# Kernel tuning notes

Measured on AMD Instinct MI355X. Metric: run time of the kernel, lower is better.

## Reference

```python
import jax, jax.numpy as jnp
import numpy as np

D_MODEL = 1024
N_HEADS = 16
HEAD_DIM = D_MODEL // N_HEADS
B, S = 4, 2048


def setup_inputs() -> dict:
    key = jax.random.key(0)
    ks = jax.random.split(key, 12)
    s = 1.0 / np.sqrt(D_MODEL)
    inp = {
        'query': jax.random.normal(ks[0], (B, S, D_MODEL), jnp.float32),
        'key': jax.random.normal(ks[1], (B, S, D_MODEL), jnp.float32),
        'value': jax.random.normal(ks[2], (B, S, D_MODEL), jnp.float32),
        # causal mask, broadcast over batch and heads: [1,1,S,S]
        'mask': jnp.tril(jnp.ones((S, S), jnp.int32))[None, None],
        'Wq': jax.random.normal(ks[3], (D_MODEL, D_MODEL), jnp.float32) * s,
        'bq': jnp.zeros((D_MODEL,), jnp.float32),
        'Wk': jax.random.normal(ks[4], (D_MODEL, D_MODEL), jnp.float32) * s,
        'bk': jnp.zeros((D_MODEL,), jnp.float32),
        'Wv': jax.random.normal(ks[5], (D_MODEL, D_MODEL), jnp.float32) * s,
        'bv': jnp.zeros((D_MODEL,), jnp.float32),
        'Wo': jax.random.normal(ks[6], (D_MODEL, D_MODEL), jnp.float32) * s,
        'bo': jnp.zeros((D_MODEL,), jnp.float32),
    }
    return inp


def reference(query, key, value, mask, Wq, bq, Wk, bk, Wv, bv, Wo, bo):
    b, q_len, _ = query.shape
    scale = jnp.sqrt(jnp.float32(HEAD_DIM))
    # projections
    q = query @ Wq + bq
    k = key @ Wk + bk
    v = value @ Wv + bv
    # [b, h, s, hd]
    q = q.reshape(b, q_len, N_HEADS, HEAD_DIM).transpose(0, 2, 1, 3)
    k = k.reshape(b, -1, N_HEADS, HEAD_DIM).transpose(0, 2, 1, 3)
    v = v.reshape(b, -1, N_HEADS, HEAD_DIM).transpose(0, 2, 1, 3)
    scores = jnp.einsum('bhqd,bhkd->bhqk', q, k) / scale
    scores = jnp.where(mask == 0, jnp.float32(-jnp.inf), scores)
    attn = jax.nn.softmax(scores, axis=-1)  # dropout p=0 / eval mode
    out = jnp.einsum('bhqk,bhkd->bhqd', attn, v)
    out = out.transpose(0, 2, 1, 3).reshape(b, q_len, D_MODEL)
    return out @ Wo + bo
```

## Files before the change

kernel.cpp:

```cpp
#include <hip/hip_runtime.h>
#include <hip/hip_bf16.h>

typedef __attribute__((ext_vector_type(8))) short short8;
typedef __attribute__((ext_vector_type(4))) float floatx4;
typedef __attribute__((ext_vector_type(4))) unsigned short ushort4v;

#define D_MODEL 1024
#define S_LEN   2048
#define N_HEADS 16
#define HEAD_DIM 64
#define BATCH   4

__device__ __forceinline__ unsigned short f2bf(float x) {
    union { float f; unsigned int u; } v; v.f = x;
    unsigned int u = v.u;
    unsigned int r = (u + 0x7FFFu + ((u >> 16) & 1u)) >> 16;
    return (unsigned short)r;
}
__device__ __forceinline__ unsigned short f2bf_trunc(float x) {
    union { float f; unsigned int u; } v; v.f = x;
    return (unsigned short)(v.u >> 16);
}

__device__ __forceinline__ void gload_lds16(const void* g, void* s) {
    __builtin_amdgcn_global_load_lds(
        (const __attribute__((address_space(1))) void*)g,
        (__attribute__((address_space(3))) void*)s, 16, 0, 0);
}

struct Conv3 {
    const float* src[3];
    unsigned short* dst[3];
};

__global__ __launch_bounds__(256) void conv_bf16(Conv3 a) {
    const float* s = a.src[blockIdx.z];
    unsigned short* d = a.dst[blockIdx.z];
    size_t i = ((size_t)blockIdx.x * 256 + threadIdx.x) * 8;
    float4 f0 = *(const float4*)(s + i);
    float4 f1 = *(const float4*)(s + i + 4);
    short8 v;
    v[0] = (short)f2bf(f0.x); v[1] = (short)f2bf(f0.y);
    v[2] = (short)f2bf(f0.z); v[3] = (short)f2bf(f0.w);
    v[4] = (short)f2bf(f1.x); v[5] = (short)f2bf(f1.y);
    v[6] = (short)f2bf(f1.z); v[7] = (short)f2bf(f1.w);
    *(short8*)(d + i) = v;
}

struct Trans4 {
    const float* W[4];
    unsigned short* Wt[4];
};

__global__ __launch_bounds__(256) void transpose_w(Trans4 args) {
    __shared__ unsigned short tile[32][33];
    const float* W = args.W[blockIdx.z];
    unsigned short* Wt = args.Wt[blockIdx.z];
    int n0 = blockIdx.x * 32;
    int k0 = blockIdx.y * 32;
    int t = threadIdx.x;
    int r = t >> 5, c = t & 31;
    for (int i = 0; i < 4; ++i) {
        int k = k0 + r + i * 8;
        tile[r + i * 8][c] = f2bf(W[(size_t)k * D_MODEL + n0 + c]);
    }
    __syncthreads();
    for (int i = 0; i < 4; ++i) {
        int n = n0 + r + i * 8;
        Wt[(size_t)n * D_MODEL + k0 + c] = tile[c][r + i * 8];
    }
}

struct GemmIn {
    const unsigned short* A;
    const unsigned short* Bt;
    const float* bias;
    void* C;
    int mode;
};
struct Gemm3 { GemmIn g[3]; };

#define BAR()   asm volatile("s_barrier" ::: "memory")
#define LGKM0() asm volatile("s_waitcnt lgkmcnt(0)" ::: "memory")
#define VMW0()  asm volatile("s_waitcnt vmcnt(0)" ::: "memory")

#define READ_A4(BUF)                                                           \
    _Pragma("unroll") for (int ii = 0; ii < 4; ++ii) {                         \
        aF[ii][0] = *(const short8*)&lds[(BUF)*16384 + aOff + ii*512];         \
        aF[ii][1] = *(const short8*)&lds[(BUF)*16384 + aOff + ii*512 + 4096];  \
    }
#define READ_B2(BUF, J0, DST)                                                  \
    _Pragma("unroll") for (int jj = 0; jj < 2; ++jj) {                         \
        DST[jj][0] = *(const short8*)&lds[(BUF)*16384 + bOff + ((J0)+jj)*512]; \
        DST[jj][1] = *(const short8*)&lds[(BUF)*16384 + bOff + ((J0)+jj)*512 + 4096]; \
    }
#define MFMA_H(J0, BREG)                                                       \
    __builtin_amdgcn_s_setprio(1);                                             \
    _Pragma("unroll") for (int ii = 0; ii < 4; ++ii)                           \
    _Pragma("unroll") for (int jj = 0; jj < 2; ++jj) {                         \
        acc[ii][(J0)+jj] = __builtin_amdgcn_mfma_f32_16x16x32_bf16(            \
            aF[ii][0], BREG[jj][0], acc[ii][(J0)+jj], 0, 0, 0);                \
        acc[ii][(J0)+jj] = __builtin_amdgcn_mfma_f32_16x16x32_bf16(            \
            aF[ii][1], BREG[jj][1], acc[ii][(J0)+jj], 0, 0, 0);                \
    }                                                                          \
    __builtin_amdgcn_s_setprio(0)

__global__ __launch_bounds__(256, 2) void gemm_128(Gemm3 args) {
    constexpr int K = D_MODEL, N = D_MODEL;
    constexpr int NT = K / 64;
    constexpr int NI = NT / 2;
    GemmIn g = args.g[blockIdx.z];

    __shared__ __align__(16) unsigned short lds[32768];

    const int m0 = blockIdx.x * 128;
    const int n0 = blockIdx.y * 128;
    const int t = threadIdx.x;
    const int w = t >> 6, lane = t & 63;
    const int quad = lane >> 4, l16 = lane & 15;
    const int wm = w >> 1, wn = w & 1;

    const int srow = w * 32 + (lane >> 2);
    const int scol = ((lane & 3) * 8) ^ ((lane & 32) ? 16 : 0);

    const int fx = (quad * 8) ^ ((l16 & 8) ? 16 : 0);
    const int aOff = (wm * 64 + l16) * 32 + fx;
    const int bOff = 8192 + (wn * 64 + l16) * 32 + fx;

    floatx4 acc[4][4] = {};
    short8 aF[4][2], bE[2][2], bO[2][2];

    auto stageA = [&](int buf, int kt) {
        const unsigned short* s0 = g.A + (size_t)(m0 + srow) * K + kt * 64 + scol;
        unsigned short* d0 = &lds[buf * 16384 + (w * 32) * 32];
        gload_lds16(s0, d0);
        gload_lds16(s0 + 32, d0 + 4096);
        gload_lds16(s0 + (size_t)16 * K, d0 + 512);
        gload_lds16(s0 + (size_t)16 * K + 32, d0 + 512 + 4096);
    };
    auto stageB = [&](int buf, int kt) {
        const unsigned short* s0 = g.Bt + (size_t)(n0 + srow) * K + kt * 64 + scol;
        unsigned short* d0 = &lds[buf * 16384 + 8192 + (w * 32) * 32];
        gload_lds16(s0, d0);
        gload_lds16(s0 + 32, d0 + 4096);
        gload_lds16(s0 + (size_t)16 * K, d0 + 512);
        gload_lds16(s0 + (size_t)16 * K + 32, d0 + 512 + 4096);
    };

    stageA(0, 0); stageB(0, 0);
    VMW0();
    BAR();

    for (int n = 0; n < NI - 1; ++n) {
        const int t0 = 2 * n;
        READ_A4(0); READ_B2(0, 0, bE);
        stageB(1, t0 + 1);
        BAR(); LGKM0();
        MFMA_H(0, bE);
        BAR();
        READ_B2(0, 2, bO);
        stageA(1, t0 + 1);
        BAR(); LGKM0();
        MFMA_H(2, bO);
        VMW0();
        BAR();
        READ_A4(1); READ_B2(1, 0, bE);
        stageB(0, t0 + 2);
        BAR(); LGKM0();
        MFMA_H(0, bE);
        BAR();
        READ_B2(1, 2, bO);
        stageA(0, t0 + 2);
        BAR(); LGKM0();
        MFMA_H(2, bO);
        VMW0();
        BAR();
    }

    {
        READ_A4(0); READ_B2(0, 0, bE);
        stageB(1, NT - 1);
        BAR(); LGKM0();
        MFMA_H(0, bE);
        BAR();
        READ_B2(0, 2, bO);
        stageA(1, NT - 1);
        BAR(); LGKM0();
        MFMA_H(2, bO);
        VMW0();
        BAR();
        READ_A4(1); READ_B2(1, 0, bE);
        BAR(); LGKM0();
        MFMA_H(0, bE);
        BAR();
        READ_B2(1, 2, bO);
        LGKM0();
        MFMA_H(2, bO);
    }

    if (g.mode == 2) {
        unsigned short* Ct = (unsigned short*)g.C;
#pragma unroll
        for (int j = 0; j < 4; ++j) {
            int col = n0 + wn * 64 + j * 16 + l16;
            int h = col >> 6, dd = col & 63;
            float bv = g.bias[col];
#pragma unroll
            for (int i = 0; i < 4; ++i) {
                int row0 = m0 + wm * 64 + i * 16 + quad * 4;
                int bb = row0 >> 11, s = row0 & 2047;
                ushort4v u;
#pragma unroll
                for (int r = 0; r < 4; ++r) u[r] = f2bf(acc[i][j][r] + bv);
                *(ushort4v*)(Ct + ((size_t)(bb * 16 + h) * 64 + dd) * 2048 + s) = u;
            }
        }
    } else {
#pragma unroll
        for (int j = 0; j < 4; ++j) {
            int col = n0 + wn * 64 + j * 16 + l16;
            float bv = g.bias[col];
#pragma unroll
            for (int i = 0; i < 4; ++i) {
#pragma unroll
                for (int r = 0; r < 4; ++r) {
                    int row = m0 + wm * 64 + i * 16 + quad * 4 + r;
                    float v = acc[i][j][r] + bv;
                    if (g.mode == 1)
                        ((float*)g.C)[(size_t)row * N + col] = v;
                    else
                        ((unsigned short*)g.C)[(size_t)row * N + col] = f2bf(v);
                }
            }
        }
    }
}

__global__ __launch_bounds__(512) void flash_attn(
    const unsigned short* __restrict__ Qp,
    const unsigned short* __restrict__ Kp,
    const unsigned short* __restrict__ Vtg,
    unsigned short* __restrict__ Op) {
    constexpr int S = S_LEN, D = D_MODEL;
    __shared__ __align__(16) unsigned short Ks[64 * 64];
    __shared__ __align__(16) unsigned short Vs[64 * 64];
    __shared__ __align__(16) unsigned short Ps[8][16][72];

    int pair = blockIdx.x;
    int bh = blockIdx.y;
    int b = bh >> 4;
    int t = threadIdx.x;
    int wave = t >> 6, lane = t & 63;
    int quad = lane >> 4, l16 = lane & 15;

    const size_t head_off = (size_t)b * S * D + (size_t)(bh & 15) * HEAD_DIM;
    const unsigned short* Khead = Kp + head_off;
    const unsigned short* Vhead = Vtg + (size_t)bh * 64 * S;

    int q0l = pair * 128, q0h = (15 - pair) * 128;
    int qgl = q0l + wave * 16 + l16;
    int qgh = q0h + wave * 16 + l16;

    const unsigned short* qpl = Qp + head_off + (size_t)qgl * D + quad * 8;
    short8 ql0 = *(const short8*)qpl, ql1 = *(const short8*)(qpl + 32);
    const unsigned short* qph = Qp + head_off + (size_t)qgh * D + quad * 8;
    short8 qh0 = *(const short8*)qph, qh1 = *(const short8*)(qph + 32);

    floatx4 ol[4] = {}, oh[4] = {};
    float ll = 0.f, lh = 0.f;
    const float cs = 0.125f * 1.44269504088896340736f;

    int sw = wave & 3;
    bool doK = wave < 4;
    int srow = sw * 16 + (lane >> 2);
    int scol = (lane & 3) * 8;
    unsigned short* sdst0 = (doK ? Ks : Vs) + sw * 512;
    unsigned short* sdst1 = sdst0 + 2048;

    int wqminl = q0l + wave * 16, wqmaxl = wqminl + 15;
    int wqminh = q0h + wave * 16, wqmaxh = wqminh + 15;

    auto half_step = [&](int k0, int qg, int wqmin, float& l_i,
                         floatx4* o, short8 qb0, short8 qb1) {
        floatx4 st[4];
        for (int gk = 0; gk < 4; ++gk) {
            short8 ka0 = *(const short8*)&Ks[(gk * 16 + l16) * 32 + quad * 8];
            short8 ka1 = *(const short8*)&Ks[2048 + (gk * 16 + l16) * 32 + quad * 8];
            floatx4 s = {};
            s = __builtin_amdgcn_mfma_f32_16x16x32_bf16(ka0, qb0, s, 0, 0, 0);
            s = __builtin_amdgcn_mfma_f32_16x16x32_bf16(ka1, qb1, s, 0, 0, 0);
            st[gk] = s;
        }

        float sv[16];
        float rs = 0.f;
        if (k0 + 63 < wqmin) {
            for (int i = 0; i < 16; ++i) {
                sv[i] = __builtin_amdgcn_exp2f(st[i >> 2][i & 3] * cs);
                rs += sv[i];
            }
        } else {
            for (int gk = 0; gk < 4; ++gk)
                for (int r = 0; r < 4; ++r) {
                    int key = k0 + gk * 16 + quad * 4 + r;
                    float p = (key <= qg)
                        ? __builtin_amdgcn_exp2f(st[gk][r] * cs) : 0.f;
                    sv[gk * 4 + r] = p;
                    rs += p;
                }
        }
        rs += __shfl_xor(rs, 16);
        rs += __shfl_xor(rs, 32);
        l_i += rs;

        for (int gk = 0; gk < 4; ++gk) {
            ushort4v u;
            for (int r = 0; r < 4; ++r) u[r] = f2bf_trunc(sv[gk * 4 + r]);
            *(ushort4v*)&Ps[wave][l16][gk * 16 + quad * 4] = u;
        }

        short8 pf0 = *(const short8*)&Ps[wave][l16][quad * 8];
        short8 pf1 = *(const short8*)&Ps[wave][l16][32 + quad * 8];
        for (int jd = 0; jd < 4; ++jd) {
            short8 va0 = *(const short8*)&Vs[(jd * 16 + l16) * 32 + quad * 8];
            short8 va1 = *(const short8*)&Vs[2048 + (jd * 16 + l16) * 32 + quad * 8];
            o[jd] = __builtin_amdgcn_mfma_f32_16x16x32_bf16(va0, pf0, o[jd], 0, 0, 0);
            o[jd] = __builtin_amdgcn_mfma_f32_16x16x32_bf16(va1, pf1, o[jd], 0, 0, 0);
        }
    };

    int n_kt = 2 * (15 - pair) + 2;
    for (int kt = 0; kt < n_kt; ++kt) {
        int k0 = kt * 64;
        if (doK) {
            gload_lds16(Khead + (size_t)(k0 + srow) * D + scol, sdst0);
            gload_lds16(Khead + (size_t)(k0 + srow) * D + 32 + scol, sdst1);
        } else {
            gload_lds16(Vhead + (size_t)srow * S + k0 + scol, sdst0);
            gload_lds16(Vhead + (size_t)srow * S + k0 + 32 + scol, sdst1);
        }
        __syncthreads();

        if (k0 <= wqmaxl) half_step(k0, qgl, wqminl, ll, ol, ql0, ql1);
        if (k0 <= wqmaxh) half_step(k0, qgh, wqminh, lh, oh, qh0, qh1);
        __syncthreads();
    }

    {
        float inv = 1.0f / ll;
        unsigned short* op = Op + head_off + (size_t)qgl * D;
        for (int jd = 0; jd < 4; ++jd) {
            ushort4v u;
            for (int r = 0; r < 4; ++r) u[r] = f2bf(ol[jd][r] * inv);
            *(ushort4v*)(op + jd * 16 + quad * 4) = u;
        }
    }
    {
        float inv = 1.0f / lh;
        unsigned short* op = Op + head_off + (size_t)qgh * D;
        for (int jd = 0; jd < 4; ++jd) {
            ushort4v u;
            for (int r = 0; r < 4; ++r) u[r] = f2bf(oh[jd][r] * inv);
            *(ushort4v*)(op + jd * 16 + quad * 4) = u;
        }
    }
}

extern "C" void kernel_launch(void* const* d_in, const int* in_sizes, int n_in,
                              void* d_out, int out_size, void* d_ws,
                              size_t ws_size, hipStream_t stream) {
    const float* query = (const float*)d_in[0];
    const float* key   = (const float*)d_in[1];
    const float* value = (const float*)d_in[2];
    const float* Wq = (const float*)d_in[4];
    const float* bq = (const float*)d_in[5];
    const float* Wk = (const float*)d_in[6];
    const float* bk = (const float*)d_in[7];
    const float* Wv = (const float*)d_in[8];
    const float* bv = (const float*)d_in[9];
    const float* Wo = (const float*)d_in[10];
    const float* bo = (const float*)d_in[11];
    float* out = (float*)d_out;

    char* ws = (char*)d_ws;
    const size_t WT_SZ = (size_t)D_MODEL * D_MODEL * 2;
    const size_t X_SZ = (size_t)BATCH * S_LEN * D_MODEL * 2;
    unsigned short* wtq = (unsigned short*)(ws);
    unsigned short* wtk = (unsigned short*)(ws + WT_SZ);
    unsigned short* wtv = (unsigned short*)(ws + 2 * WT_SZ);
    unsigned short* wto = (unsigned short*)(ws + 3 * WT_SZ);
    unsigned short* Qbf = (unsigned short*)(ws + 4 * WT_SZ);
    unsigned short* Kbf = (unsigned short*)(ws + 4 * WT_SZ + X_SZ);
    unsigned short* Vbf = (unsigned short*)(ws + 4 * WT_SZ + 2 * X_SZ);
    unsigned short* Qp  = (unsigned short*)(ws + 4 * WT_SZ + 3 * X_SZ);
    unsigned short* Kp  = (unsigned short*)(ws + 4 * WT_SZ + 4 * X_SZ);
    unsigned short* Vtg = (unsigned short*)(ws + 4 * WT_SZ + 5 * X_SZ);
    unsigned short* Ao  = Qbf;

    Trans4 ta;
    ta.W[0] = Wq; ta.W[1] = Wk; ta.W[2] = Wv; ta.W[3] = Wo;
    ta.Wt[0] = wtq; ta.Wt[1] = wtk; ta.Wt[2] = wtv; ta.Wt[3] = wto;
    transpose_w<<<dim3(32, 32, 4), 256, 0, stream>>>(ta);

    Conv3 ca;
    ca.src[0] = query; ca.src[1] = key; ca.src[2] = value;
    ca.dst[0] = Qbf;   ca.dst[1] = Kbf; ca.dst[2] = Vbf;
    conv_bf16<<<dim3(4096, 1, 3), 256, 0, stream>>>(ca);

    Gemm3 gq;
    gq.g[0].A = Qbf; gq.g[0].Bt = wtq; gq.g[0].bias = bq; gq.g[0].C = Qp;  gq.g[0].mode = 0;
    gq.g[1].A = Kbf; gq.g[1].Bt = wtk; gq.g[1].bias = bk; gq.g[1].C = Kp;  gq.g[1].mode = 0;
    gq.g[2].A = Vbf; gq.g[2].Bt = wtv; gq.g[2].bias = bv; gq.g[2].C = Vtg; gq.g[2].mode = 2;
    gemm_128<<<dim3(64, 8, 3), 256, 0, stream>>>(gq);

    flash_attn<<<dim3(8, BATCH * N_HEADS), 512, 0, stream>>>(
        Qp, Kp, Vtg, Ao);

    Gemm3 go;
    go.g[0].A = Ao; go.g[0].Bt = wto; go.g[0].bias = bo; go.g[0].C = out; go.g[0].mode = 1;
    gemm_128<<<dim3(64, 8, 1), 256, 0, stream>>>(go);
}
```

Before: 329.8 us.

## Double-buffer K/V tiles in flash attention with swizzled LDS layout

Splits the K/V LDS staging into two buffers so the global-to-LDS load of the next key tile is issued before computing on the current one, waiting with a partial vmcnt instead of a full sync. Adds an XOR swizzle to the K, V and P LDS layouts to reduce bank conflicts, and raises wave priority around the MFMA blocks. The cost is double the K/V LDS footprint, which may lower occupancy. The swizzle has to match between the staging writes and the fragment reads, so any mismatch would give wrong results.

```diff
diff --git a/kernel.cpp b/kernel.cpp
--- a/kernel.cpp
+++ b/kernel.cpp
@@ -82,6 +82,7 @@
 
 #define BAR()   asm volatile("s_barrier" ::: "memory")
 #define LGKM0() asm volatile("s_waitcnt lgkmcnt(0)" ::: "memory")
+#define VMW2()  asm volatile("s_waitcnt vmcnt(2)" ::: "memory")
 #define VMW0()  asm volatile("s_waitcnt vmcnt(0)" ::: "memory")
 
 #define READ_A4(BUF)                                                           \
@@ -242,9 +243,9 @@
     const unsigned short* __restrict__ Vtg,
     unsigned short* __restrict__ Op) {
     constexpr int S = S_LEN, D = D_MODEL;
-    __shared__ __align__(16) unsigned short Ks[64 * 64];
-    __shared__ __align__(16) unsigned short Vs[64 * 64];
-    __shared__ __align__(16) unsigned short Ps[8][16][72];
+    __shared__ __align__(16) unsigned short Ks[2 * 4096];
+    __shared__ __align__(16) unsigned short Vs[2 * 4096];
+    __shared__ __align__(16) unsigned short Ps[8][1024];
 
     int pair = blockIdx.x;
     int bh = blockIdx.y;
@@ -273,24 +274,43 @@
     int sw = wave & 3;
     bool doK = wave < 4;
     int srow = sw * 16 + (lane >> 2);
-    int scol = (lane & 3) * 8;
-    unsigned short* sdst0 = (doK ? Ks : Vs) + sw * 512;
-    unsigned short* sdst1 = sdst0 + 2048;
+    int scol = ((lane & 3) * 8) ^ ((lane & 32) ? 16 : 0);
+
+    auto stage = [&](int buf, int k0) {
+        if (doK) {
+            const unsigned short* s0 = Khead + (size_t)(k0 + srow) * D + scol;
+            unsigned short* d0 = Ks + buf * 4096 + sw * 512;
+            gload_lds16(s0, d0);
+            gload_lds16(s0 + 32, d0 + 2048);
+        } else {
+            const unsigned short* s0 = Vhead + (size_t)srow * S + k0 + scol;
+            unsigned short* d0 = Vs + buf * 4096 + sw * 512;
+            gload_lds16(s0, d0);
+            gload_lds16(s0 + 32, d0 + 2048);
+        }
+    };
 
     int wqminl = q0l + wave * 16, wqmaxl = wqminl + 15;
     int wqminh = q0h + wave * 16, wqmaxh = wqminh + 15;
 
-    auto half_step = [&](int k0, int qg, int wqmin, float& l_i,
+    const int swz = (quad * 8) ^ ((l16 & 8) ? 16 : 0);
+    const int pswz = (l16 & 8) ? 16 : 0;
+    unsigned short* pw = &Ps[wave][0];
+
+    auto half_step = [&](const unsigned short* Kb, const unsigned short* Vb,
+                         int k0, int qg, int wqmin, float& l_i,
                          floatx4* o, short8 qb0, short8 qb1) {
         floatx4 st[4];
+        __builtin_amdgcn_s_setprio(1);
         for (int gk = 0; gk < 4; ++gk) {
-            short8 ka0 = *(const short8*)&Ks[(gk * 16 + l16) * 32 + quad * 8];
-            short8 ka1 = *(const short8*)&Ks[2048 + (gk * 16 + l16) * 32 + quad * 8];
+            short8 ka0 = *(const short8*)&Kb[(gk * 16 + l16) * 32 + swz];
+            short8 ka1 = *(const short8*)&Kb[2048 + (gk * 16 + l16) * 32 + swz];
             floatx4 s = {};
             s = __builtin_amdgcn_mfma_f32_16x16x32_bf16(ka0, qb0, s, 0, 0, 0);
             s = __builtin_amdgcn_mfma_f32_16x16x32_bf16(ka1, qb1, s, 0, 0, 0);
             st[gk] = s;
         }
+        __builtin_amdgcn_s_setprio(0);
 
         float sv[16];
         float rs = 0.f;
@@ -316,34 +336,39 @@
         for (int gk = 0; gk < 4; ++gk) {
             ushort4v u;
             for (int r = 0; r < 4; ++r) u[r] = f2bf_trunc(sv[gk * 4 + r]);
-            *(ushort4v*)&Ps[wave][l16][gk * 16 + quad * 4] = u;
-        }
-
-        short8 pf0 = *(const short8*)&Ps[wave][l16][quad * 8];
-        short8 pf1 = *(const short8*)&Ps[wave][l16][32 + quad * 8];
+            *(ushort4v*)&pw[(gk >> 1) * 512 + l16 * 32 +
+                            ((((gk & 1) * 16) + quad * 4) ^ pswz)] = u;
+        }
+
+        short8 pf0 = *(const short8*)&pw[l16 * 32 + swz];
+        short8 pf1 = *(const short8*)&pw[512 + l16 * 32 + swz];
+        __builtin_amdgcn_s_setprio(1);
         for (int jd = 0; jd < 4; ++jd) {
-            short8 va0 = *(const short8*)&Vs[(jd * 16 + l16) * 32 + quad * 8];
-            short8 va1 = *(const short8*)&Vs[2048 + (jd * 16 + l16) * 32 + quad * 8];
+            short8 va0 = *(const short8*)&Vb[(jd * 16 + l16) * 32 + swz];
+            short8 va1 = *(const short8*)&Vb[2048 + (jd * 16 + l16) * 32 + swz];
             o[jd] = __builtin_amdgcn_mfma_f32_16x16x32_bf16(va0, pf0, o[jd], 0, 0, 0);
             o[jd] = __builtin_amdgcn_mfma_f32_16x16x32_bf16(va1, pf1, o[jd], 0, 0, 0);
         }
+        __builtin_amdgcn_s_setprio(0);
     };
 
     int n_kt = 2 * (15 - pair) + 2;
+    stage(0, 0);
     for (int kt = 0; kt < n_kt; ++kt) {
         int k0 = kt * 64;
-        if (doK) {
-            gload_lds16(Khead + (size_t)(k0 + srow) * D + scol, sdst0);
-            gload_lds16(Khead + (size_t)(k0 + srow) * D + 32 + scol, sdst1);
+        if (kt + 1 < n_kt) {
+            stage((kt + 1) & 1, k0 + 64);
+            VMW2();
         } else {
-            gload_lds16(Vhead + (size_t)srow * S + k0 + scol, sdst0);
-            gload_lds16(Vhead + (size_t)srow * S + k0 + 32 + scol, sdst1);
-        }
-        __syncthreads();
-
-        if (k0 <= wqmaxl) half_step(k0, qgl, wqminl, ll, ol, ql0, ql1);
-        if (k0 <= wqmaxh) half_step(k0, qgh, wqminh, lh, oh, qh0, qh1);
-        __syncthreads();
+            VMW0();
+        }
+        BAR();
+
+        const unsigned short* Kb = Ks + (kt & 1) * 4096;
+        const unsigned short* Vb = Vs + (kt & 1) * 4096;
+        if (k0 <= wqmaxl) half_step(Kb, Vb, k0, qgl, wqminl, ll, ol, ql0, ql1);
+        if (k0 <= wqmaxh) half_step(Kb, Vb, k0, qgh, wqminh, lh, oh, qh0, qh1);
+        BAR();
     }
 
     {
```

Result: faster. 304.8 us (-7.6%).
